# Kernel tuning notes

Measured on AMD Instinct MI355X. Metric: run time of the kernel, lower is better.

Reference implementation:

```python
import jax, jax.numpy as jnp
import numpy as np
from math import sqrt

HEADS = 16
DIM_HEAD = 64
BETA = 1.0 / sqrt(DIM_HEAD)


def setup_inputs() -> dict:
    key = jax.random.key(0)
    k1, k2, k3 = jax.random.split(key, 3)
    b, n, dim = 2, 2048, 1024
    inner = HEADS * DIM_HEAD  # 1024
    x = jax.random.normal(k1, (b, n, dim), dtype=jnp.float32)
    W_qk = jax.random.normal(k2, (dim, 2 * inner), dtype=jnp.float32) * 0.02
    W_out = jax.random.normal(k3, (inner, dim), dtype=jnp.float32) * 0.02
    return {"x": x, "W_qk": W_qk, "W_out": W_out}


def reference(x, W_qk, W_out):
    # x: [b, n, dim]; to_qk: Linear(dim, 2*inner, bias=False)
    b, n, _ = x.shape
    qk = x @ W_qk                                   # [b, n, 2*inner]
    q, k = jnp.split(qk, 2, axis=-1)                # each [b, n, inner]
    # b n (h d) -> b h n d
    q = q.reshape(b, n, HEADS, DIM_HEAD).transpose(0, 2, 1, 3)
    k = k.reshape(b, n, HEADS, DIM_HEAD).transpose(0, 2, 1, 3)
    # beta-scaled scores
    scores = jnp.einsum('bhid,bhjd->bhij', q * BETA, k)  # [b, h, n, n]
    mask_value = -jnp.finfo(scores.dtype).max
    causal_mask = jnp.triu(jnp.ones((n, n), dtype=bool), k=1)
    scores = jnp.where(causal_mask, mask_value, scores)
    attn = jax.nn.softmax(scores, axis=-1)
    # K is reused as V
    out = jnp.einsum('bhij,bhjd->bhid', attn, k)    # [b, h, n, d]
    out = out.transpose(0, 2, 1, 3).reshape(b, n, HEADS * DIM_HEAD)
    # to_out Linear (dropout is identity in eval)
    return out @ W_out
```

## Files before the change

kernel.cpp:

```cpp
#include <hip/hip_runtime.h>
#include <hip/hip_bf16.h>
#include <math.h>

typedef short bf16x8 __attribute__((ext_vector_type(8)));
typedef float f32x4 __attribute__((ext_vector_type(4)));

__device__ __forceinline__ float bf2f(unsigned short u) {
    return __uint_as_float(((unsigned int)u) << 16);
}
__device__ __forceinline__ unsigned short f2bf(float f) {
    unsigned int u = __float_as_uint(f);
    u = (u + 0x7FFFu + ((u >> 16) & 1u)) >> 16;
    return (unsigned short)u;
}

#define ASYNC16(gp, lp)                                                        \
    __builtin_amdgcn_global_load_lds(                                          \
        (const __attribute__((address_space(1))) unsigned int*)(gp),           \
        (__attribute__((address_space(3))) unsigned int*)(lp), 16, 0, 0)

__global__ __launch_bounds__(256) void cast_x_kernel(const float* __restrict__ in,
                                                     unsigned short* __restrict__ out, int n) {
    int i = (blockIdx.x * 256 + threadIdx.x) * 8;
    if (i >= n) return;
    float4 a = *(const float4*)(in + i);
    float4 b = *(const float4*)(in + i + 4);
    bf16x8 v;
    v[0] = (short)f2bf(a.x); v[1] = (short)f2bf(a.y); v[2] = (short)f2bf(a.z); v[3] = (short)f2bf(a.w);
    v[4] = (short)f2bf(b.x); v[5] = (short)f2bf(b.y); v[6] = (short)f2bf(b.z); v[7] = (short)f2bf(b.w);
    *(bf16x8*)(out + i) = v;
}

__global__ __launch_bounds__(256) void transpose_cast_kernel(const float* __restrict__ in,
                                                             unsigned short* __restrict__ out,
                                                             int K, int N) {
    __shared__ float tile[32][33];
    int k0 = blockIdx.x * 32, n0 = blockIdx.y * 32;
    int tx = threadIdx.x & 31, ty = threadIdx.x >> 5;
    #pragma unroll
    for (int i = ty; i < 32; i += 8)
        tile[i][tx] = in[(size_t)(k0 + i) * N + (n0 + tx)];
    __syncthreads();
    #pragma unroll
    for (int i = ty; i < 32; i += 8)
        out[(size_t)(n0 + i) * K + (k0 + tx)] = f2bf(tile[tx][i]);
}

__global__ __launch_bounds__(256) void ktrans_kernel(const unsigned short* __restrict__ qkb,
                                                     unsigned short* __restrict__ kT) {
    __shared__ unsigned short tl[64][68];
    const int b = blockIdx.z;
    const int tok0 = blockIdx.x * 64;
    const int f0 = blockIdx.y * 64;
    const int r = threadIdx.x >> 4;
    const int c = (threadIdx.x & 15) * 4;
    #pragma unroll
    for (int i = 0; i < 4; ++i) {
        const int rr = r + 16 * i;
        ushort4 v = *(const ushort4*)(qkb + ((size_t)(b * 2048 + tok0 + rr)) * 2048 + 1024 + f0 + c);
        *(ushort4*)&tl[rr][c] = v;
    }
    __syncthreads();
    #pragma unroll
    for (int i = 0; i < 4; ++i) {
        const int fr = r + 16 * i;
        ushort4 v;
        v.x = tl[c + 0][fr]; v.y = tl[c + 1][fr]; v.z = tl[c + 2][fr]; v.w = tl[c + 3][fr];
        *(ushort4*)(kT + ((size_t)(b * 1024 + f0 + fr)) * 2048 + tok0 + c) = v;
    }
}

template <bool STORE_BF16>
__global__ __launch_bounds__(256) void gemm128_kernel(const unsigned short* __restrict__ A,
                                                      const unsigned short* __restrict__ Bt,
                                                      void* __restrict__ C,
                                                      int K, int lda, int ldb, int ldc) {
    __shared__ unsigned short As[128 * 32];
    __shared__ unsigned short Bs[128 * 32];
    const int tid = threadIdx.x;
    const int wave = tid >> 6;
    const int lane = tid & 63;
    const int quad = lane >> 4;
    const int col  = lane & 15;
    const int wm = (wave >> 1) * 64;
    const int wn = (wave & 1) * 64;
    const int m0 = blockIdx.x * 128, n0 = blockIdx.y * 128;

    f32x4 acc[4][4];
    #pragma unroll
    for (int i = 0; i < 4; ++i)
        #pragma unroll
        for (int j = 0; j < 4; ++j) { acc[i][j][0] = 0.f; acc[i][j][1] = 0.f; acc[i][j][2] = 0.f; acc[i][j][3] = 0.f; }

    const int srow = tid >> 2;
    const int skc  = (tid & 3) * 8;

    for (int k0 = 0; k0 < K; k0 += 32) {
        __syncthreads();
        const unsigned short* ga = A  + (size_t)(m0 + srow) * lda + k0 + skc;
        const unsigned short* gb = Bt + (size_t)(n0 + srow) * ldb + k0 + skc;
        ASYNC16(ga,            &As[wave * 512]);
        ASYNC16(ga + 64 * lda, &As[2048 + wave * 512]);
        ASYNC16(gb,            &Bs[wave * 512]);
        ASYNC16(gb + 64 * ldb, &Bs[2048 + wave * 512]);
        __syncthreads();

        bf16x8 af[4], bf[4];
        #pragma unroll
        for (int mf = 0; mf < 4; ++mf)
            af[mf] = *(const bf16x8*)&As[(wm + mf * 16 + col) * 32 + quad * 8];
        #pragma unroll
        for (int nf = 0; nf < 4; ++nf)
            bf[nf] = *(const bf16x8*)&Bs[(wn + nf * 16 + col) * 32 + quad * 8];
        #pragma unroll
        for (int mf = 0; mf < 4; ++mf)
            #pragma unroll
            for (int nf = 0; nf < 4; ++nf)
                acc[mf][nf] = __builtin_amdgcn_mfma_f32_16x16x32_bf16(af[mf], bf[nf], acc[mf][nf], 0, 0, 0);
    }

    #pragma unroll
    for (int mf = 0; mf < 4; ++mf) {
        const int row0 = m0 + wm + mf * 16 + quad * 4;
        #pragma unroll
        for (int nf = 0; nf < 4; ++nf) {
            const int cc = n0 + wn + nf * 16 + col;
            #pragma unroll
            for (int r = 0; r < 4; ++r) {
                if (STORE_BF16)
                    ((unsigned short*)C)[(size_t)(row0 + r) * ldc + cc] = f2bf(acc[mf][nf][r]);
                else
                    ((float*)C)[(size_t)(row0 + r) * ldc + cc] = acc[mf][nf][r];
            }
        }
    }
}

#define LDK 72

__global__ __launch_bounds__(256) void attn_v3_kernel(const unsigned short* __restrict__ qkb,
                                                      const unsigned short* __restrict__ kT,
                                                      unsigned short* __restrict__ aout) {
    __shared__ unsigned short Kn[64 * 64];
    __shared__ unsigned short Kt[64 * 64];
    __shared__ unsigned short Ps[4][16 * LDK];

    const int bh = blockIdx.x;
    const int b = bh >> 4, h = bh & 15;
    const int qtile = 31 - (int)blockIdx.y;
    const int tid = threadIdx.x;
    const int wave = tid >> 6, lane = tid & 63, quad = lane >> 4, col = lane & 15;

    bf16x8 qa0, qa1;
    {
        const unsigned short* qp =
            qkb + ((size_t)(b * 2048 + qtile * 64 + wave * 16 + col)) * 2048 + h * 64;
        bf16x8 r0 = *(const bf16x8*)(qp + quad * 8);
        bf16x8 r1 = *(const bf16x8*)(qp + 32 + quad * 8);
        const float sc = 0.125f * 1.44269504088896f;
        #pragma unroll
        for (int i = 0; i < 8; ++i) {
            qa0[i] = (short)f2bf(bf2f((unsigned short)r0[i]) * sc);
            qa1[i] = (short)f2bf(bf2f((unsigned short)r1[i]) * sc);
        }
    }

    f32x4 accO[4];
    #pragma unroll
    for (int t = 0; t < 4; ++t) { accO[t][0] = 0.f; accO[t][1] = 0.f; accO[t][2] = 0.f; accO[t][3] = 0.f; }
    float lsum = 0.f;

    const int r8 = lane >> 3;
    const int c8 = (lane & 7) ^ r8;
    const unsigned short* knp =
        qkb + ((size_t)(b * 2048 + wave * 16 + r8)) * 2048 + 1024 + h * 64 + c8 * 8;
    const unsigned short* ktp = kT + ((size_t)(bh * 64 + wave * 16 + r8)) * 2048 + c8 * 8;
    unsigned short* const knl0 = &Kn[(wave * 16) * 64];
    unsigned short* const knl1 = &Kn[(wave * 16 + 8) * 64];
    unsigned short* const ktl0 = &Kt[(wave * 16) * 64];
    unsigned short* const ktl1 = &Kt[(wave * 16 + 8) * 64];

    for (int jt = 0; jt <= qtile; ++jt) {
        __syncthreads();
        ASYNC16(knp,            knl0);
        ASYNC16(knp + 8 * 2048, knl1);
        ASYNC16(ktp,            ktl0);
        ASYNC16(ktp + 8 * 2048, ktl1);
        knp += 64 * 2048;
        ktp += 64;
        __syncthreads();

        const bool diag = (jt == qtile);
        const int tmax = diag ? wave : 3;

        float ls = 0.f;
        unsigned int pw[4][2];
        #pragma unroll
        for (int t = 0; t < 4; ++t) {
            if (t <= tmax) {
                const int row = (t * 16 + col) * 64;
                const int sw = col & 7;
                bf16x8 ka0 = *(const bf16x8*)&Kn[row + (quad ^ sw) * 8];
                bf16x8 ka1 = *(const bf16x8*)&Kn[row + ((4 + quad) ^ sw) * 8];
                f32x4 c = {-16.f, -16.f, -16.f, -16.f};
                c = __builtin_amdgcn_mfma_f32_16x16x32_bf16(ka0, qa0, c, 0, 0, 0);
                c = __builtin_amdgcn_mfma_f32_16x16x32_bf16(ka1, qa1, c, 0, 0, 0);
                if (diag && t == wave) {
                    #pragma unroll
                    for (int r = 0; r < 4; ++r)
                        if (quad * 4 + r > col) c[r] = -1e30f;
                }
                const float p0 = exp2f(c[0]);
                const float p1 = exp2f(c[1]);
                const float p2 = exp2f(c[2]);
                const float p3 = exp2f(c[3]);
                ls += (p0 + p1) + (p2 + p3);
                __hip_bfloat162 u0 = __float22bfloat162_rn(make_float2(p0, p1));
                __hip_bfloat162 u1 = __float22bfloat162_rn(make_float2(p2, p3));
                pw[t][0] = *(unsigned int*)&u0;
                pw[t][1] = *(unsigned int*)&u1;
            } else {
                pw[t][0] = 0u; pw[t][1] = 0u;
            }
        }
        lsum += ls;

        unsigned short* psb = &Ps[wave][col * LDK];
        #pragma unroll
        for (int t = 0; t < 4; ++t)
            *(uint2*)(psb + t * 16 + quad * 4) = make_uint2(pw[t][0], pw[t][1]);

        bf16x8 pa0 = *(const bf16x8*)(psb + quad * 8);
        bf16x8 pa1 = *(const bf16x8*)(psb + 32 + quad * 8);
        const bool hi = !(diag && wave < 2);

        #pragma unroll
        for (int t = 0; t < 4; ++t) {
            const int row = (t * 16 + col) * 64;
            const int sw = col & 7;
            bf16x8 vb0 = *(const bf16x8*)&Kt[row + (quad ^ sw) * 8];
            accO[t] = __builtin_amdgcn_mfma_f32_16x16x32_bf16(pa0, vb0, accO[t], 0, 0, 0);
            if (hi) {
                bf16x8 vb1 = *(const bf16x8*)&Kt[row + ((4 + quad) ^ sw) * 8];
                accO[t] = __builtin_amdgcn_mfma_f32_16x16x32_bf16(pa1, vb1, accO[t], 0, 0, 0);
            }
        }
    }

    lsum += __shfl_xor(lsum, 16);
    lsum += __shfl_xor(lsum, 32);
    #pragma unroll
    for (int r = 0; r < 4; ++r) {
        const float lr = __shfl(lsum, (lane & 48) | (quad * 4 + r));
        const float inv = 1.f / lr;
        const size_t row = (size_t)b * 2048 + qtile * 64 + wave * 16 + quad * 4 + r;
        unsigned short* op = aout + row * 1024 + h * 64;
        op[col]      = f2bf(accO[0][r] * inv);
        op[16 + col] = f2bf(accO[1][r] * inv);
        op[32 + col] = f2bf(accO[2][r] * inv);
        op[48 + col] = f2bf(accO[3][r] * inv);
    }
}

extern "C" void kernel_launch(void* const* d_in, const int* in_sizes, int n_in,
                              void* d_out, int out_size, void* d_ws, size_t ws_size,
                              hipStream_t stream) {
    (void)in_sizes; (void)n_in; (void)out_size; (void)ws_size;
    const float* x    = (const float*)d_in[0];
    const float* Wqk  = (const float*)d_in[1];
    const float* Wout = (const float*)d_in[2];
    float* out = (float*)d_out;

    unsigned short* xb     = (unsigned short*)d_ws;
    unsigned short* Wqk_t  = xb     + (size_t)4096 * 1024;
    unsigned short* Wout_t = Wqk_t  + (size_t)2048 * 1024;
    unsigned short* qkb    = Wout_t + (size_t)1024 * 1024;
    unsigned short* aoutb  = qkb    + (size_t)4096 * 2048;
    unsigned short* kT     = xb;

    cast_x_kernel<<<dim3(4096 * 1024 / (256 * 8)), dim3(256), 0, stream>>>(x, xb, 4096 * 1024);
    transpose_cast_kernel<<<dim3(32, 64), dim3(256), 0, stream>>>(Wqk, Wqk_t, 1024, 2048);
    transpose_cast_kernel<<<dim3(32, 32), dim3(256), 0, stream>>>(Wout, Wout_t, 1024, 1024);

    gemm128_kernel<true><<<dim3(32, 16), dim3(256), 0, stream>>>(
        xb, Wqk_t, (void*)qkb, 1024, 1024, 1024, 2048);

    ktrans_kernel<<<dim3(32, 16, 2), dim3(256), 0, stream>>>(qkb, kT);

    attn_v3_kernel<<<dim3(32, 32), dim3(256), 0, stream>>>(qkb, kT, aoutb);

    gemm128_kernel<false><<<dim3(32, 8), dim3(256), 0, stream>>>(
        aoutb, Wout_t, (void*)out, 1024, 1024, 1024, 1024);
}
```

Before: 195.1 us.

## Fuse x fp32-to-bf16 cast into QK GEMM and halve attention query tile

Drops the separate cast_x kernel: the QK projection GEMM now reads fp32 x directly, converts it to bf16 in registers and writes it to padded LDS, which saves one launch and a full bf16 round trip of x through memory. The attention kernel switches to 32-query tiles with 128-thread blocks, doubling the grid so causal work spreads across more CUs with less idle time. The trade-off is that the fp32 A path loads synchronously instead of through async global-to-LDS copies, and each attention block now loads every K tile for half as many queries.

```diff
diff --git a/kernel.cpp b/kernel.cpp
--- a/kernel.cpp
+++ b/kernel.cpp
@@ -13,23 +13,15 @@
     u = (u + 0x7FFFu + ((u >> 16) & 1u)) >> 16;
     return (unsigned short)u;
 }
+__device__ __forceinline__ unsigned int pk2bf(float a, float b) {
+    __hip_bfloat162 u = __float22bfloat162_rn(make_float2(a, b));
+    return *(unsigned int*)&u;
+}
 
 #define ASYNC16(gp, lp)                                                        \
     __builtin_amdgcn_global_load_lds(                                          \
         (const __attribute__((address_space(1))) unsigned int*)(gp),           \
         (__attribute__((address_space(3))) unsigned int*)(lp), 16, 0, 0)
-
-__global__ __launch_bounds__(256) void cast_x_kernel(const float* __restrict__ in,
-                                                     unsigned short* __restrict__ out, int n) {
-    int i = (blockIdx.x * 256 + threadIdx.x) * 8;
-    if (i >= n) return;
-    float4 a = *(const float4*)(in + i);
-    float4 b = *(const float4*)(in + i + 4);
-    bf16x8 v;
-    v[0] = (short)f2bf(a.x); v[1] = (short)f2bf(a.y); v[2] = (short)f2bf(a.z); v[3] = (short)f2bf(a.w);
-    v[4] = (short)f2bf(b.x); v[5] = (short)f2bf(b.y); v[6] = (short)f2bf(b.z); v[7] = (short)f2bf(b.w);
-    *(bf16x8*)(out + i) = v;
-}
 
 __global__ __launch_bounds__(256) void transpose_cast_kernel(const float* __restrict__ in,
                                                              unsigned short* __restrict__ out,
@@ -70,12 +62,13 @@
     }
 }
 
-template <bool STORE_BF16>
-__global__ __launch_bounds__(256) void gemm128_kernel(const unsigned short* __restrict__ A,
+template <bool STORE_BF16, bool A_FP32>
+__global__ __launch_bounds__(256) void gemm128_kernel(const void* __restrict__ Av,
                                                       const unsigned short* __restrict__ Bt,
                                                       void* __restrict__ C,
                                                       int K, int lda, int ldb, int ldc) {
-    __shared__ unsigned short As[128 * 32];
+    constexpr int ASTR = A_FP32 ? 40 : 32;
+    __shared__ unsigned short As[128 * ASTR];
     __shared__ unsigned short Bs[128 * 32];
     const int tid = threadIdx.x;
     const int wave = tid >> 6;
@@ -94,13 +87,29 @@
 
     const int srow = tid >> 2;
     const int skc  = (tid & 3) * 8;
+    const int frow = tid >> 1;
+    const int fcol = (tid & 1) * 16;
 
     for (int k0 = 0; k0 < K; k0 += 32) {
         __syncthreads();
-        const unsigned short* ga = A  + (size_t)(m0 + srow) * lda + k0 + skc;
+        if (A_FP32) {
+            const float* gx = (const float*)Av + (size_t)(m0 + frow) * lda + k0 + fcol;
+            float4 f0 = *(const float4*)(gx);
+            float4 f1 = *(const float4*)(gx + 4);
+            float4 f2 = *(const float4*)(gx + 8);
+            float4 f3 = *(const float4*)(gx + 12);
+            uint4 w0 = make_uint4(pk2bf(f0.x, f0.y), pk2bf(f0.z, f0.w),
+                                  pk2bf(f1.x, f1.y), pk2bf(f1.z, f1.w));
+            uint4 w1 = make_uint4(pk2bf(f2.x, f2.y), pk2bf(f2.z, f2.w),
+                                  pk2bf(f3.x, f3.y), pk2bf(f3.z, f3.w));
+            *(uint4*)&As[frow * ASTR + fcol]     = w0;
+            *(uint4*)&As[frow * ASTR + fcol + 8] = w1;
+        } else {
+            const unsigned short* ga = (const unsigned short*)Av + (size_t)(m0 + srow) * lda + k0 + skc;
+            ASYNC16(ga,            &As[wave * 512]);
+            ASYNC16(ga + 64 * lda, &As[2048 + wave * 512]);
+        }
         const unsigned short* gb = Bt + (size_t)(n0 + srow) * ldb + k0 + skc;
-        ASYNC16(ga,            &As[wave * 512]);
-        ASYNC16(ga + 64 * lda, &As[2048 + wave * 512]);
         ASYNC16(gb,            &Bs[wave * 512]);
         ASYNC16(gb + 64 * ldb, &Bs[2048 + wave * 512]);
         __syncthreads();
@@ -108,7 +117,7 @@
         bf16x8 af[4], bf[4];
         #pragma unroll
         for (int mf = 0; mf < 4; ++mf)
-            af[mf] = *(const bf16x8*)&As[(wm + mf * 16 + col) * 32 + quad * 8];
+            af[mf] = *(const bf16x8*)&As[(wm + mf * 16 + col) * ASTR + quad * 8];
         #pragma unroll
         for (int nf = 0; nf < 4; ++nf)
             bf[nf] = *(const bf16x8*)&Bs[(wn + nf * 16 + col) * 32 + quad * 8];
@@ -138,23 +147,24 @@
 
 #define LDK 72
 
-__global__ __launch_bounds__(256) void attn_v3_kernel(const unsigned short* __restrict__ qkb,
+__global__ __launch_bounds__(128) void attn_v4_kernel(const unsigned short* __restrict__ qkb,
                                                       const unsigned short* __restrict__ kT,
                                                       unsigned short* __restrict__ aout) {
     __shared__ unsigned short Kn[64 * 64];
     __shared__ unsigned short Kt[64 * 64];
-    __shared__ unsigned short Ps[4][16 * LDK];
+    __shared__ unsigned short Ps[2][16 * LDK];
 
     const int bh = blockIdx.x;
     const int b = bh >> 4, h = bh & 15;
-    const int qtile = 31 - (int)blockIdx.y;
+    const int qt = 63 - (int)blockIdx.y;
     const int tid = threadIdx.x;
     const int wave = tid >> 6, lane = tid & 63, quad = lane >> 4, col = lane & 15;
+    const int Q0 = qt * 32;
 
     bf16x8 qa0, qa1;
     {
         const unsigned short* qp =
-            qkb + ((size_t)(b * 2048 + qtile * 64 + wave * 16 + col)) * 2048 + h * 64;
+            qkb + ((size_t)(b * 2048 + Q0 + wave * 16 + col)) * 2048 + h * 64;
         bf16x8 r0 = *(const bf16x8*)(qp + quad * 8);
         bf16x8 r1 = *(const bf16x8*)(qp + 32 + quad * 8);
         const float sc = 0.125f * 1.44269504088896f;
@@ -173,25 +183,28 @@
     const int r8 = lane >> 3;
     const int c8 = (lane & 7) ^ r8;
     const unsigned short* knp =
-        qkb + ((size_t)(b * 2048 + wave * 16 + r8)) * 2048 + 1024 + h * 64 + c8 * 8;
-    const unsigned short* ktp = kT + ((size_t)(bh * 64 + wave * 16 + r8)) * 2048 + c8 * 8;
-    unsigned short* const knl0 = &Kn[(wave * 16) * 64];
-    unsigned short* const knl1 = &Kn[(wave * 16 + 8) * 64];
-    unsigned short* const ktl0 = &Kt[(wave * 16) * 64];
-    unsigned short* const ktl1 = &Kt[(wave * 16 + 8) * 64];
-
-    for (int jt = 0; jt <= qtile; ++jt) {
+        qkb + ((size_t)(b * 2048 + wave * 32 + r8)) * 2048 + 1024 + h * 64 + c8 * 8;
+    const unsigned short* ktp = kT + ((size_t)(bh * 64 + wave * 32 + r8)) * 2048 + c8 * 8;
+    unsigned short* const knl = &Kn[(wave * 32) * 64];
+    unsigned short* const ktl = &Kt[(wave * 32) * 64];
+
+    const int jtd = qt >> 1;
+    const int qoff = (qt & 1) * 32 + wave * 16;
+    const int tdiag = qoff >> 4;
+
+    for (int jt = 0; jt <= jtd; ++jt) {
         __syncthreads();
-        ASYNC16(knp,            knl0);
-        ASYNC16(knp + 8 * 2048, knl1);
-        ASYNC16(ktp,            ktl0);
-        ASYNC16(ktp + 8 * 2048, ktl1);
+        #pragma unroll
+        for (int g = 0; g < 4; ++g) {
+            ASYNC16(knp + g * 8 * 2048, knl + g * 8 * 64);
+            ASYNC16(ktp + g * 8 * 2048, ktl + g * 8 * 64);
+        }
         knp += 64 * 2048;
         ktp += 64;
         __syncthreads();
 
-        const bool diag = (jt == qtile);
-        const int tmax = diag ? wave : 3;
+        const bool diag = (jt == jtd);
+        const int tmax = diag ? tdiag : 3;
 
         float ls = 0.f;
         unsigned int pw[4][2];
@@ -205,7 +218,7 @@
                 f32x4 c = {-16.f, -16.f, -16.f, -16.f};
                 c = __builtin_amdgcn_mfma_f32_16x16x32_bf16(ka0, qa0, c, 0, 0, 0);
                 c = __builtin_amdgcn_mfma_f32_16x16x32_bf16(ka1, qa1, c, 0, 0, 0);
-                if (diag && t == wave) {
+                if (diag && t == tdiag) {
                     #pragma unroll
                     for (int r = 0; r < 4; ++r)
                         if (quad * 4 + r > col) c[r] = -1e30f;
@@ -215,10 +228,8 @@
                 const float p2 = exp2f(c[2]);
                 const float p3 = exp2f(c[3]);
                 ls += (p0 + p1) + (p2 + p3);
-                __hip_bfloat162 u0 = __float22bfloat162_rn(make_float2(p0, p1));
-                __hip_bfloat162 u1 = __float22bfloat162_rn(make_float2(p2, p3));
-                pw[t][0] = *(unsigned int*)&u0;
-                pw[t][1] = *(unsigned int*)&u1;
+                pw[t][0] = pk2bf(p0, p1);
+                pw[t][1] = pk2bf(p2, p3);
             } else {
                 pw[t][0] = 0u; pw[t][1] = 0u;
             }
@@ -232,7 +243,7 @@
 
         bf16x8 pa0 = *(const bf16x8*)(psb + quad * 8);
         bf16x8 pa1 = *(const bf16x8*)(psb + 32 + quad * 8);
-        const bool hi = !(diag && wave < 2);
+        const bool hi = !(diag && tdiag < 2);
 
         #pragma unroll
         for (int t = 0; t < 4; ++t) {
@@ -253,7 +264,7 @@
     for (int r = 0; r < 4; ++r) {
         const float lr = __shfl(lsum, (lane & 48) | (quad * 4 + r));
         const float inv = 1.f / lr;
-        const size_t row = (size_t)b * 2048 + qtile * 64 + wave * 16 + quad * 4 + r;
+        const size_t row = (size_t)b * 2048 + Q0 + wave * 16 + quad * 4 + r;
         unsigned short* op = aout + row * 1024 + h * 64;
         op[col]      = f2bf(accO[0][r] * inv);
         op[16 + col] = f2bf(accO[1][r] * inv);
@@ -271,24 +282,22 @@
     const float* Wout = (const float*)d_in[2];
     float* out = (float*)d_out;
 
-    unsigned short* xb     = (unsigned short*)d_ws;
-    unsigned short* Wqk_t  = xb     + (size_t)4096 * 1024;
+    unsigned short* kT     = (unsigned short*)d_ws;
+    unsigned short* Wqk_t  = kT     + (size_t)4096 * 1024;
     unsigned short* Wout_t = Wqk_t  + (size_t)2048 * 1024;
     unsigned short* qkb    = Wout_t + (size_t)1024 * 1024;
     unsigned short* aoutb  = qkb    + (size_t)4096 * 2048;
-    unsigned short* kT     = xb;
-
-    cast_x_kernel<<<dim3(4096 * 1024 / (256 * 8)), dim3(256), 0, stream>>>(x, xb, 4096 * 1024);
+
     transpose_cast_kernel<<<dim3(32, 64), dim3(256), 0, stream>>>(Wqk, Wqk_t, 1024, 2048);
     transpose_cast_kernel<<<dim3(32, 32), dim3(256), 0, stream>>>(Wout, Wout_t, 1024, 1024);
 
-    gemm128_kernel<true><<<dim3(32, 16), dim3(256), 0, stream>>>(
-        xb, Wqk_t, (void*)qkb, 1024, 1024, 1024, 2048);
+    gemm128_kernel<true, true><<<dim3(32, 16), dim3(256), 0, stream>>>(
+        (const void*)x, Wqk_t, (void*)qkb, 1024, 1024, 1024, 2048);
 
     ktrans_kernel<<<dim3(32, 16, 2), dim3(256), 0, stream>>>(qkb, kT);
 
-    attn_v3_kernel<<<dim3(32, 32), dim3(256), 0, stream>>>(qkb, kT, aoutb);
-
-    gemm128_kernel<false><<<dim3(32, 8), dim3(256), 0, stream>>>(
-        aoutb, Wout_t, (void*)out, 1024, 1024, 1024, 1024);
-}
+    attn_v4_kernel<<<dim3(32, 64), dim3(128), 0, stream>>>(qkb, kT, aoutb);
+
+    gemm128_kernel<false, false><<<dim3(32, 8), dim3(256), 0, stream>>>(
+        (const void*)aoutb, Wout_t, (void*)out, 1024, 1024, 1024, 1024);
+}
```

New measurement: 203.3 us. +4.2%, slower.

## Double-buffer K tiles in attention kernel with async prefetch of next tile

Applied to the files above, without the earlier changes.

The attention kernel now keeps two LDS buffers for the K and K-transposed tiles and issues the async global-to-LDS loads for tile jt+1 before computing on tile jt. A partial vmcnt wait lets the current tile's loads complete while the next tile's loads stay in flight. This aims to hide global load latency behind the MFMA and exp work. In exchange LDS use doubles, which may lower occupancy, and correctness depends on hand-coded waitcnt encodings and raw barriers.

```diff
diff --git a/kernel.cpp b/kernel.cpp
--- a/kernel.cpp
+++ b/kernel.cpp
@@ -12,6 +12,10 @@
     unsigned int u = __float_as_uint(f);
     u = (u + 0x7FFFu + ((u >> 16) & 1u)) >> 16;
     return (unsigned short)u;
+}
+__device__ __forceinline__ unsigned int pk2bf(float a, float b) {
+    __hip_bfloat162 u = __float22bfloat162_rn(make_float2(a, b));
+    return *(unsigned int*)&u;
 }
 
 #define ASYNC16(gp, lp)                                                        \
@@ -138,11 +142,10 @@
 
 #define LDK 72
 
-__global__ __launch_bounds__(256) void attn_v3_kernel(const unsigned short* __restrict__ qkb,
+__global__ __launch_bounds__(256) void attn_v5_kernel(const unsigned short* __restrict__ qkb,
                                                       const unsigned short* __restrict__ kT,
                                                       unsigned short* __restrict__ aout) {
-    __shared__ unsigned short Kn[64 * 64];
-    __shared__ unsigned short Kt[64 * 64];
+    __shared__ unsigned short Kbuf[2][2][64 * 64];
     __shared__ unsigned short Ps[4][16 * LDK];
 
     const int bh = blockIdx.x;
@@ -175,20 +178,31 @@
     const unsigned short* knp =
         qkb + ((size_t)(b * 2048 + wave * 16 + r8)) * 2048 + 1024 + h * 64 + c8 * 8;
     const unsigned short* ktp = kT + ((size_t)(bh * 64 + wave * 16 + r8)) * 2048 + c8 * 8;
-    unsigned short* const knl0 = &Kn[(wave * 16) * 64];
-    unsigned short* const knl1 = &Kn[(wave * 16 + 8) * 64];
-    unsigned short* const ktl0 = &Kt[(wave * 16) * 64];
-    unsigned short* const ktl1 = &Kt[(wave * 16 + 8) * 64];
+
+    auto issue = [&](int jt, int p) {
+        const unsigned short* kn = knp + (size_t)jt * 64 * 2048;
+        const unsigned short* kt = ktp + jt * 64;
+        unsigned short* knl = &Kbuf[p][0][(wave * 16) * 64];
+        unsigned short* ktl = &Kbuf[p][1][(wave * 16) * 64];
+        ASYNC16(kn,            knl);
+        ASYNC16(kn + 8 * 2048, knl + 8 * 64);
+        ASYNC16(kt,            ktl);
+        ASYNC16(kt + 8 * 2048, ktl + 8 * 64);
+    };
+
+    issue(0, 0);
 
     for (int jt = 0; jt <= qtile; ++jt) {
-        __syncthreads();
-        ASYNC16(knp,            knl0);
-        ASYNC16(knp + 8 * 2048, knl1);
-        ASYNC16(ktp,            ktl0);
-        ASYNC16(ktp + 8 * 2048, ktl1);
-        knp += 64 * 2048;
-        ktp += 64;
-        __syncthreads();
+        const int cur = jt & 1;
+        __builtin_amdgcn_s_barrier();
+        if (jt < qtile) issue(jt + 1, cur ^ 1);
+        if (jt < qtile) __builtin_amdgcn_s_waitcnt(0xF74);
+        else            __builtin_amdgcn_s_waitcnt(0xF70);
+        __builtin_amdgcn_s_barrier();
+        __asm__ volatile("" ::: "memory");
+
+        const unsigned short* Knc = &Kbuf[cur][0][0];
+        const unsigned short* Ktc = &Kbuf[cur][1][0];
 
         const bool diag = (jt == qtile);
         const int tmax = diag ? wave : 3;
@@ -200,8 +214,8 @@
             if (t <= tmax) {
                 const int row = (t * 16 + col) * 64;
                 const int sw = col & 7;
-                bf16x8 ka0 = *(const bf16x8*)&Kn[row + (quad ^ sw) * 8];
-                bf16x8 ka1 = *(const bf16x8*)&Kn[row + ((4 + quad) ^ sw) * 8];
+                bf16x8 ka0 = *(const bf16x8*)&Knc[row + (quad ^ sw) * 8];
+                bf16x8 ka1 = *(const bf16x8*)&Knc[row + ((4 + quad) ^ sw) * 8];
                 f32x4 c = {-16.f, -16.f, -16.f, -16.f};
                 c = __builtin_amdgcn_mfma_f32_16x16x32_bf16(ka0, qa0, c, 0, 0, 0);
                 c = __builtin_amdgcn_mfma_f32_16x16x32_bf16(ka1, qa1, c, 0, 0, 0);
@@ -215,10 +229,8 @@
                 const float p2 = exp2f(c[2]);
                 const float p3 = exp2f(c[3]);
                 ls += (p0 + p1) + (p2 + p3);
-                __hip_bfloat162 u0 = __float22bfloat162_rn(make_float2(p0, p1));
-                __hip_bfloat162 u1 = __float22bfloat162_rn(make_float2(p2, p3));
-                pw[t][0] = *(unsigned int*)&u0;
-                pw[t][1] = *(unsigned int*)&u1;
+                pw[t][0] = pk2bf(p0, p1);
+                pw[t][1] = pk2bf(p2, p3);
             } else {
                 pw[t][0] = 0u; pw[t][1] = 0u;
             }
@@ -238,10 +250,10 @@
         for (int t = 0; t < 4; ++t) {
             const int row = (t * 16 + col) * 64;
             const int sw = col & 7;
-            bf16x8 vb0 = *(const bf16x8*)&Kt[row + (quad ^ sw) * 8];
+            bf16x8 vb0 = *(const bf16x8*)&Ktc[row + (quad ^ sw) * 8];
             accO[t] = __builtin_amdgcn_mfma_f32_16x16x32_bf16(pa0, vb0, accO[t], 0, 0, 0);
             if (hi) {
-                bf16x8 vb1 = *(const bf16x8*)&Kt[row + ((4 + quad) ^ sw) * 8];
+                bf16x8 vb1 = *(const bf16x8*)&Ktc[row + ((4 + quad) ^ sw) * 8];
                 accO[t] = __builtin_amdgcn_mfma_f32_16x16x32_bf16(pa1, vb1, accO[t], 0, 0, 0);
             }
         }
@@ -287,7 +299,7 @@
 
     ktrans_kernel<<<dim3(32, 16, 2), dim3(256), 0, stream>>>(qkb, kT);
 
-    attn_v3_kernel<<<dim3(32, 32), dim3(256), 0, stream>>>(qkb, kT, aoutb);
+    attn_v5_kernel<<<dim3(32, 32), dim3(256), 0, stream>>>(qkb, kT, aoutb);
 
     gemm128_kernel<false><<<dim3(32, 8), dim3(256), 0, stream>>>(
         aoutb, Wout_t, (void*)out, 1024, 1024, 1024, 1024);
```

Measured after the change: 194.8 us. No clear change (-0.1%).
